# Kernel tuning notes

Hardware: AMD Instinct MI355X
Metric: run time of the kernel (lower is better)

Reference implementation:

```python
import jax, jax.numpy as jnp
import numpy as np

B, C, H, W = 8, 256, 128, 128
N = H * W
TEMP = 0.07
NUM_NEG = 128
HARD_RADIUS = 4
HARD_RATIO = 0.75   # curriculum fully ramped (_current_hard_ratio == hard_ratio_max)
N_HARD = int(NUM_NEG * HARD_RATIO)   # 96
N_RAND = NUM_NEG - N_HARD            # 32
STEP = max(1, H // 16)               # 8
N_POS = ((H + STEP - 1) // STEP) * ((W + STEP - 1) // STEP)  # 256


def setup_inputs() -> dict:
    key = jax.random.key(0)
    ks = jax.random.split(key, 8)
    fmap_rgb = jax.random.normal(ks[0], (B, C, H, W), jnp.float32)
    fmap_depth = jax.random.normal(ks[1], (B, C, H, W), jnp.float32)
    pu = jax.random.uniform(ks[2], (B, H, W), jnp.float32) * (W - 1)
    pv = jax.random.uniform(ks[3], (B, H, W), jnp.float32) * (H - 1)
    projected_coords = jnp.stack([pu, pv], axis=1)  # (B,2,H,W)
    valid_mask = (jax.random.uniform(ks[4], (B, H, W)) < 0.9).astype(jnp.float32)
    rand_idx = jax.random.randint(ks[5], (B, N_RAND), 0, N, dtype=jnp.int32)
    hard_off_u = jax.random.randint(ks[6], (B, N_HARD, N_POS), -HARD_RADIUS, HARD_RADIUS + 1, dtype=jnp.int32)
    hard_off_v = jax.random.randint(ks[7], (B, N_HARD, N_POS), -HARD_RADIUS, HARD_RADIUS + 1, dtype=jnp.int32)
    return {
        'fmap_rgb': fmap_rgb, 'fmap_depth': fmap_depth,
        'projected_coords': projected_coords, 'valid_mask': valid_mask,
        'rand_idx': rand_idx, 'hard_off_u': hard_off_u, 'hard_off_v': hard_off_v,
    }


def _normalize(x):
    # F.normalize(dim=1): x / max(||x||_2, eps)
    n = jnp.sqrt(jnp.sum(x * x, axis=1, keepdims=True))
    return x / jnp.maximum(n, 1e-12)


def _bilinear_sample(f, x, y):
    # grid_sample(mode=bilinear, padding=zeros, align_corners=True); unnormalized
    # coords equal pixel coords (x=proj_u, y=proj_v). f:(B,C,H,W), x,y:(B,H,W) -> (B,C,N)
    Bb, Cc, Hh, Ww = f.shape
    ff = f.reshape(Bb, Cc, Hh * Ww)
    xf = x.reshape(Bb, -1)
    yf = y.reshape(Bb, -1)
    x0 = jnp.floor(xf)
    y0 = jnp.floor(yf)
    wx = xf - x0
    wy = yf - y0
    x0i = x0.astype(jnp.int32)
    y0i = y0.astype(jnp.int32)

    def g(ix, iy):
        valid = (ix >= 0) & (ix < Ww) & (iy >= 0) & (iy < Hh)
        idx = jnp.clip(iy, 0, Hh - 1) * Ww + jnp.clip(ix, 0, Ww - 1)
        v = jnp.take_along_axis(ff, idx[:, None, :], axis=2)
        return v * valid[:, None, :]

    return (((1 - wx) * (1 - wy))[:, None, :] * g(x0i, y0i)
            + (wx * (1 - wy))[:, None, :] * g(x0i + 1, y0i)
            + ((1 - wx) * wy)[:, None, :] * g(x0i, y0i + 1)
            + (wx * wy)[:, None, :] * g(x0i + 1, y0i + 1))


def reference(fmap_rgb, fmap_depth, projected_coords, valid_mask, rand_idx, hard_off_u, hard_off_v):
    rgb = _normalize(fmap_rgb)
    dep = _normalize(fmap_depth)
    proj_u = projected_coords[:, 0]
    proj_v = projected_coords[:, 1]

    rgb_pos = _bilinear_sample(rgb, proj_u, proj_v)        # (B,C,N)
    dep_flat = dep.reshape(B, C, N)
    rgb_flat = rgb.reshape(B, C, N)
    pos_sim = jnp.sum(dep_flat * rgb_pos, axis=1) / TEMP    # (B,N)

    # random negatives via gather + batched matmul
    rgb_rand = jnp.take_along_axis(rgb_flat, rand_idx[:, None, :].astype(jnp.int32), axis=2)  # (B,C,n_rand)
    rand_neg = jnp.einsum('bcn,bck->bkn', dep_flat, rgb_rand) / TEMP  # (B,n_rand,N)

    # hard negatives on coarse grid (step = H//16)
    gh = jnp.arange(0, H, STEP)
    gw = jnp.arange(0, W, STEP)
    ghf, gwf = [a.reshape(-1) for a in jnp.meshgrid(gh, gw, indexing='ij')]
    grid_idx = ghf * W + gwf                                # (n_pos,)
    pos_u = jnp.clip(proj_u[:, ghf, gwf], 0, W - 1).astype(jnp.int32)  # (B,n_pos)
    pos_v = jnp.clip(proj_v[:, ghf, gwf], 0, H - 1).astype(jnp.int32)
    off_u = jnp.where((hard_off_u == 0) & (hard_off_v == 0), 1, hard_off_u)
    hu = jnp.clip(pos_u[:, None, :] + off_u, 0, W - 1)      # (B,n_hard,n_pos)
    hv = jnp.clip(pos_v[:, None, :] + hard_off_v, 0, H - 1)
    hard_idx = (hv * W + hu).reshape(B, -1)                 # (B, n_hard*n_pos)
    rgb_hard = jnp.take_along_axis(rgb_flat, hard_idx[:, None, :], axis=2).reshape(B, C, N_HARD, N_POS)
    dep_grid = dep_flat[:, :, grid_idx]                     # (B,C,n_pos)
    hard_sim = jnp.einsum('bcp,bchp->bhp', dep_grid, rgb_hard) / TEMP  # (B,n_hard,n_pos)

    # logsumexp over [pos; random negs; hard negs] -- hard negs only exist at grid
    # positions (the torch code scatters into a dense -inf (B,n_hard,N) tensor;
    # logaddexp at grid positions is mathematically identical and avoids it).
    lse_base = jax.scipy.special.logsumexp(
        jnp.concatenate([pos_sim[:, None, :], rand_neg], axis=1), axis=1)  # (B,N)
    lse_hard = jax.scipy.special.logsumexp(hard_sim, axis=1)               # (B,n_pos)
    lse = lse_base.at[:, grid_idx].set(jnp.logaddexp(lse_base[:, grid_idx], lse_hard))

    mask = valid_mask.reshape(B, N)
    denom = jnp.maximum(jnp.sum(mask), 1.0)
    loss = jnp.sum((lse - pos_sim) * mask) / denom

    # accuracy (no_grad in torch); max over all negatives, hard ones only at grid idx
    max_neg = jnp.max(rand_neg, axis=1)
    max_neg = max_neg.at[:, grid_idx].max(jnp.max(hard_sim, axis=1))
    correct = ((pos_sim > max_neg) & (mask > 0.5)).astype(jnp.float32)
    accuracy = jnp.sum(correct) / denom * 100.0
    return loss, jax.lax.stop_gradient(accuracy)
```

## Files before the change

kernel.cpp:

```cpp
#include <hip/hip_runtime.h>
#include <cfloat>
#include <math.h>

#define B_ 8
#define C_ 256
#define C2_ (C_/2)
#define H_ 128
#define W_ 128
#define N_ (H_*W_)
#define NRAND 32
#define NHARD 96
#define NPOS 256
#define INV_TEMP (1.0f/0.07f)

typedef __attribute__((ext_vector_type(8))) short short8;
typedef __attribute__((ext_vector_type(4))) float f32x4;

__device__ __forceinline__ unsigned bf16rne(float x) {
    unsigned u = __float_as_uint(x);
    return (u + 0x7FFFu + ((u >> 16) & 1u)) >> 16;
}
__device__ __forceinline__ float blo(unsigned w) { return __uint_as_float(w << 16); }
__device__ __forceinline__ float bhi(unsigned w) { return __uint_as_float(w & 0xFFFF0000u); }

__global__ __launch_bounds__(256) void k1_rgb_norm_T(const float* __restrict__ rgb,
                                                     unsigned* __restrict__ rgbT) {
    __shared__ __align__(16) uint4 bounce[64 * 32];
    __shared__ float red[4][64];
    __shared__ float invn[64];
    int bi = blockIdx.x;
    int b  = bi >> 8;
    int p0 = (bi & 255) << 6;
    int t  = threadIdx.x;
    int lane = t & 63, w = t >> 6;

    const float* src = rgb + (size_t)b * C_ * N_ + p0 + lane;
    float v[64];
    float ssq = 0.f;
    #pragma unroll
    for (int k = 0; k < 64; ++k) {
        v[k] = src[(size_t)(w * 64 + k) * N_];
        ssq += v[k] * v[k];
    }
    red[w][lane] = ssq;
    __syncthreads();
    if (t < 64) {
        float s = red[0][t] + red[1][t] + red[2][t] + red[3][t];
        invn[t] = 1.0f / fmaxf(sqrtf(s), 1e-12f);
    }
    __syncthreads();
    float sc = invn[lane];
    int swz = lane & 7;
    #pragma unroll
    for (int j = 0; j < 8; ++j) {
        uint4 q;
        q.x = bf16rne(v[8 * j + 0] * sc) | (bf16rne(v[8 * j + 1] * sc) << 16);
        q.y = bf16rne(v[8 * j + 2] * sc) | (bf16rne(v[8 * j + 3] * sc) << 16);
        q.z = bf16rne(v[8 * j + 4] * sc) | (bf16rne(v[8 * j + 5] * sc) << 16);
        q.w = bf16rne(v[8 * j + 6] * sc) | (bf16rne(v[8 * j + 7] * sc) << 16);
        bounce[lane * 32 + ((w * 8 + j) ^ swz)] = q;
    }
    __syncthreads();
    uint4* dst = (uint4*)(rgbT + (size_t)(b * N_ + p0) * C2_);
    #pragma unroll
    for (int it = 0; it < 8; ++it) {
        int idx = it * 256 + t;
        int px = idx >> 5, j = idx & 31;
        dst[idx] = bounce[px * 32 + (j ^ (px & 7))];
    }
}

__global__ __launch_bounds__(256) void k2_main(
        const float* __restrict__ dep, const unsigned* __restrict__ rgbT,
        const float* __restrict__ coords, const int* __restrict__ rand_idx,
        float* __restrict__ lse_base, float* __restrict__ pos_out,
        float* __restrict__ maxneg_out, unsigned* __restrict__ depG) {
    __shared__ __align__(16) uint4 dep4[64 * 32];
    __shared__ __align__(16) uint4 rs4[32 * 32];
    __shared__ float red[4][64];
    __shared__ float invn[64];
    int bi = blockIdx.x;
    int b  = bi >> 8;
    int p0 = (bi & 255) << 6;
    int t  = threadIdx.x;
    int lane = t & 63, w = t >> 6;

    #pragma unroll
    for (int it = 0; it < 4; ++it) {
        int flat = it * 256 + t;
        int rn = flat >> 5, c8 = flat & 31;
        int idx = rand_idx[b * NRAND + rn];
        const uint4* src = (const uint4*)(rgbT + (size_t)(b * N_ + idx) * C2_);
        rs4[rn * 32 + (c8 ^ (rn & 7))] = src[c8];
    }

    const float* depb = dep + (size_t)b * C_ * N_ + p0 + lane;
    float ssq = 0.f;
    int psw = lane & 7;
    #pragma unroll 2
    for (int i = 0; i < 8; ++i) {
        int c0 = w * 64 + i * 8;
        float v[8];
        #pragma unroll
        for (int k = 0; k < 8; ++k) {
            v[k] = depb[(size_t)(c0 + k) * N_];
            ssq += v[k] * v[k];
        }
        uint4 q;
        q.x = bf16rne(v[0]) | (bf16rne(v[1]) << 16);
        q.y = bf16rne(v[2]) | (bf16rne(v[3]) << 16);
        q.z = bf16rne(v[4]) | (bf16rne(v[5]) << 16);
        q.w = bf16rne(v[6]) | (bf16rne(v[7]) << 16);
        dep4[lane * 32 + ((w * 8 + i) ^ psw)] = q;
    }
    red[w][lane] = ssq;

    int px = t >> 2, g = t & 3;
    int n  = p0 + px;
    float xf = coords[(size_t)b * 2 * N_ + n];
    float yf = coords[(size_t)b * 2 * N_ + N_ + n];
    float x0 = floorf(xf), y0 = floorf(yf);
    float wx = xf - x0, wy = yf - y0;
    int ix = (int)x0 + (g & 1);
    int iy = (int)y0 + (g >> 1);
    float wgt = ((g & 1) ? wx : 1.f - wx) * ((g & 2) ? wy : 1.f - wy);
    if (ix < 0 || ix >= W_ || iy < 0 || iy >= H_) wgt = 0.f;
    int ixc = min(max(ix, 0), W_ - 1), iyc = min(max(iy, 0), H_ - 1);
    const uint4* nbr4 = (const uint4*)(rgbT + (size_t)(b * N_ + iyc * W_ + ixc) * C2_);

    __syncthreads();
    if (t < 64) {
        float s = red[0][t] + red[1][t] + red[2][t] + red[3][t];
        invn[t] = 1.0f / fmaxf(sqrtf(s), 1e-12f);
    }

    f32x4 acc0 = {0.f, 0.f, 0.f, 0.f};
    f32x4 acc1 = {0.f, 0.f, 0.f, 0.f};
    int l15 = lane & 15, l4 = lane >> 4;
    int pxA = (w << 4) + l15;
    const short8* lds8 = (const short8*)dep4;
    const short8* rnd8 = (const short8*)rs4;
    #pragma unroll
    for (int kc = 0; kc < 8; ++kc) {
        int c8 = kc * 4 + l4;
        short8 a  = lds8[pxA * 32 + (c8 ^ (pxA & 7))];
        short8 b0 = rnd8[l15 * 32 + (c8 ^ (l15 & 7))];
        short8 b1 = rnd8[(16 + l15) * 32 + (c8 ^ (l15 & 7))];
        acc0 = __builtin_amdgcn_mfma_f32_16x16x32_bf16(a, b0, acc0, 0, 0, 0);
        acc1 = __builtin_amdgcn_mfma_f32_16x16x32_bf16(a, b1, acc1, 0, 0, 0);
    }

    float accN = 0.f;
    const uint4* drow = dep4 + (size_t)px * 32;
    int dsw = px & 7;
    #pragma unroll 4
    for (int c8 = 0; c8 < 32; ++c8) {
        uint4 dq = drow[c8 ^ dsw];
        uint4 rq = nbr4[c8];
        accN += blo(dq.x) * blo(rq.x) + bhi(dq.x) * bhi(rq.x)
              + blo(dq.y) * blo(rq.y) + bhi(dq.y) * bhi(rq.y)
              + blo(dq.z) * blo(rq.z) + bhi(dq.z) * bhi(rq.z)
              + blo(dq.w) * blo(rq.w) + bhi(dq.w) * bhi(rq.w);
    }
    __syncthreads();

    float* simsF = (float*)rs4;
    #pragma unroll
    for (int r = 0; r < 4; ++r) {
        int prow = (w << 4) + (l4 << 2) + r;
        int swn = r << 2;
        simsF[prow * 32 + (l15 ^ swn)]        = acc0[r];
        simsF[prow * 32 + (16 + (l15 ^ swn))] = acc1[r];
    }
    __syncthreads();

    float scale = invn[px] * INV_TEMP;
    float pp = accN * wgt;
    pp += __shfl_xor(pp, 1, 4);
    pp += __shfl_xor(pp, 2, 4);
    float pos = pp * scale;
    const float4* sf = (const float4*)simsF;
    int fsw = px & 3;
    float4 ra = sf[px * 8 + ((g * 2) ^ fsw)];
    float4 rb = sf[px * 8 + (((g * 2) ^ fsw) ^ 1)];
    float r[8] = {ra.x, ra.y, ra.z, ra.w, rb.x, rb.y, rb.z, rb.w};
    float ml = -FLT_MAX;
    #pragma unroll
    for (int j = 0; j < 8; ++j) { r[j] *= scale; ml = fmaxf(ml, r[j]); }
    ml = fmaxf(ml, __shfl_xor(ml, 1, 4));
    ml = fmaxf(ml, __shfl_xor(ml, 2, 4));
    float mneg = ml;
    float mall = fmaxf(mneg, pos);
    float se = 0.f;
    #pragma unroll
    for (int j = 0; j < 8; ++j) se += expf(r[j] - mall);
    se += __shfl_xor(se, 1, 4);
    se += __shfl_xor(se, 2, 4);
    if (g == 0) {
        float lse = mall + logf(se + expf(pos - mall));
        size_t o = (size_t)b * N_ + n;
        lse_base[o]   = lse;
        pos_out[o]    = pos;
        maxneg_out[o] = mneg;
    }

    int y = p0 >> 7;
    if ((y & 7) == 0) {
        int m = t >> 5, u = t & 31;
        int gpx = m * 8;
        int gx  = (p0 & 127) + gpx;
        int p   = ((y >> 3) << 4) + (gx >> 3);
        float sc = invn[gpx];
        const unsigned* srow = (const unsigned*)(dep4 + (size_t)gpx * 32);
        int xsw = (gpx & 7) << 2;
        unsigned* dst = depG + (size_t)((b << 8) + p) * 128;
        #pragma unroll
        for (int it = 0; it < 4; ++it) {
            int uu = u + it * 32;
            unsigned wv = srow[uu ^ xsw];
            dst[uu] = bf16rne(blo(wv) * sc) | (bf16rne(bhi(wv) * sc) << 16);
        }
    }
}

__global__ __launch_bounds__(192) void k3_hard(
        const unsigned* __restrict__ depG, const unsigned* __restrict__ rgbT,
        const float* __restrict__ coords, const int* __restrict__ hoffu,
        const int* __restrict__ hoffv, float* __restrict__ lse_hard,
        float* __restrict__ max_hard) {
    __shared__ __align__(16) float dv[256];
    __shared__ float sm_[3], ss_[3];
    int bp = blockIdx.x;
    int b = bp >> 8, p = bp & 255;
    int gy = (p >> 4) * 8, gx = (p & 15) * 8;
    int nn = gy * W_ + gx;
    int t  = threadIdx.x;
    if (t < 128) {
        unsigned wv = depG[(size_t)bp * 128 + t];
        dv[2 * t]     = blo(wv);
        dv[2 * t + 1] = bhi(wv);
    }
    float pu = coords[(size_t)b * 2 * N_ + nn];
    float pv = coords[(size_t)b * 2 * N_ + N_ + nn];
    int iu = (int)fminf(fmaxf(pu, 0.f), (float)(W_ - 1));
    int iv = (int)fminf(fmaxf(pv, 0.f), (float)(H_ - 1));
    int h = t >> 1, half = t & 1;
    int ou = hoffu[((size_t)b * NHARD + h) * NPOS + p];
    int ov = hoffv[((size_t)b * NHARD + h) * NPOS + p];
    __syncthreads();
    if (ou == 0 && ov == 0) ou = 1;
    int hu = min(max(iu + ou, 0), W_ - 1);
    int hv = min(max(iv + ov, 0), H_ - 1);
    const uint4* hvec = (const uint4*)(rgbT + (size_t)(b * N_ + hv * W_ + hu) * C2_)
                        + half * 16;
    const float4* dvv = (const float4*)dv + half * 32;
    float acc = 0.f;
    #pragma unroll 4
    for (int c8 = 0; c8 < 16; ++c8) {
        uint4 q = hvec[c8];
        float4 d0 = dvv[c8 * 2];
        float4 d1 = dvv[c8 * 2 + 1];
        acc += d0.x * blo(q.x) + d0.y * bhi(q.x)
             + d0.z * blo(q.y) + d0.w * bhi(q.y)
             + d1.x * blo(q.z) + d1.y * bhi(q.z)
             + d1.z * blo(q.w) + d1.w * bhi(q.w);
    }
    float sim = (acc + __shfl_xor(acc, 1, 2)) * INV_TEMP;
    float m = sim;
    #pragma unroll
    for (int o = 32; o > 0; o >>= 1) m = fmaxf(m, __shfl_xor(m, o, 64));
    int wid = t >> 6;
    if ((t & 63) == 0) sm_[wid] = m;
    __syncthreads();
    float mm = fmaxf(fmaxf(sm_[0], sm_[1]), sm_[2]);
    float e = (half == 0) ? expf(sim - mm) : 0.f;
    #pragma unroll
    for (int o = 32; o > 0; o >>= 1) e += __shfl_xor(e, o, 64);
    if ((t & 63) == 0) ss_[wid] = e;
    __syncthreads();
    if (t == 0) {
        lse_hard[bp] = mm + logf(ss_[0] + ss_[1] + ss_[2]);
        max_hard[bp] = mm;
    }
}

__global__ __launch_bounds__(256) void k4_reduce(
        const float* __restrict__ lse_base, const float* __restrict__ pos_sim,
        const float* __restrict__ max_neg, const float* __restrict__ mask,
        const float* __restrict__ lse_hard, const float* __restrict__ max_hard,
        float* __restrict__ acc) {
    int i = blockIdx.x * 256 + threadIdx.x;
    float l  = lse_base[i], ps = pos_sim[i], mn = max_neg[i], mk = mask[i];
    int b = i >> 14;
    int n = i & (N_ - 1);
    int y = n >> 7, x = n & 127;
    if (((y & 7) | (x & 7)) == 0) {
        int p = ((y >> 3) << 4) + (x >> 3);
        float lh = lse_hard[(b << 8) + p];
        float mh = max_hard[(b << 8) + p];
        float m = fmaxf(l, lh);
        l  = m + logf(expf(l - m) + expf(lh - m));
        mn = fmaxf(mn, mh);
    }
    float s0 = (l - ps) * mk;
    float s1 = (ps > mn && mk > 0.5f) ? 1.f : 0.f;
    float s2 = mk;
    #pragma unroll
    for (int o = 32; o > 0; o >>= 1) {
        s0 += __shfl_down(s0, o, 64);
        s1 += __shfl_down(s1, o, 64);
        s2 += __shfl_down(s2, o, 64);
    }
    __shared__ float r0[4], r1[4], r2[4];
    int wid = threadIdx.x >> 6;
    if ((threadIdx.x & 63) == 0) { r0[wid] = s0; r1[wid] = s1; r2[wid] = s2; }
    __syncthreads();
    if (threadIdx.x == 0) {
        atomicAdd(&acc[0], r0[0] + r0[1] + r0[2] + r0[3]);
        atomicAdd(&acc[1], r1[0] + r1[1] + r1[2] + r1[3]);
        atomicAdd(&acc[2], r2[0] + r2[1] + r2[2] + r2[3]);
    }
}

__global__ void k5_final(const float* __restrict__ acc, float* __restrict__ out) {
    if (threadIdx.x == 0) {
        float denom = fmaxf(acc[2], 1.0f);
        out[0] = acc[0] / denom;
        out[1] = acc[1] / denom * 100.0f;
    }
}

extern "C" void kernel_launch(void* const* d_in, const int* in_sizes, int n_in,
                              void* d_out, int out_size, void* d_ws, size_t ws_size,
                              hipStream_t stream) {
    const float* rgb     = (const float*)d_in[0];
    const float* dep     = (const float*)d_in[1];
    const float* coords  = (const float*)d_in[2];
    const float* mask    = (const float*)d_in[3];
    const int*   rand_i  = (const int*)d_in[4];
    const int*   hoffu   = (const int*)d_in[5];
    const int*   hoffv   = (const int*)d_in[6];
    float* out = (float*)d_out;
    char*  ws  = (char*)d_ws;

    const size_t RGBT_B = (size_t)B_ * N_ * C_ * 2;
    const size_t PIX_B  = (size_t)B_ * N_ * 4;
    unsigned* rgbT  = (unsigned*)ws;
    float* lse_base = (float*)(ws + RGBT_B);
    float* pos_sim  = (float*)(ws + RGBT_B + PIX_B);
    float* max_neg  = (float*)(ws + RGBT_B + 2 * PIX_B);
    float* lse_hard = (float*)(ws + RGBT_B + 3 * PIX_B);
    float* max_hard = (float*)(ws + RGBT_B + 3 * PIX_B + 8192);
    float* acc      = (float*)(ws + RGBT_B + 3 * PIX_B + 2 * 8192);
    unsigned* depG  = (unsigned*)(ws + RGBT_B + 3 * PIX_B + 2 * 8192 + 1024);

    hipMemsetAsync(acc, 0, 16, stream);
    k1_rgb_norm_T<<<B_ * (N_ / 64), 256, 0, stream>>>(rgb, rgbT);
    k2_main<<<B_ * (N_ / 64), 256, 0, stream>>>(dep, rgbT, coords, rand_i,
                                                lse_base, pos_sim, max_neg, depG);
    k3_hard<<<B_ * NPOS, 192, 0, stream>>>(depG, rgbT, coords, hoffu, hoffv,
                                           lse_hard, max_hard);
    k4_reduce<<<(B_ * N_) / 256, 256, 0, stream>>>(lse_base, pos_sim, max_neg,
                                                   mask, lse_hard, max_hard, acc);
    k5_final<<<1, 64, 0, stream>>>(acc, out);
}
```

Before: 371.8 us.

## Fuse hard-negative, reduction and finalize kernels into one launch

Merges the hard-negative scoring kernel, the per-pixel reduction kernel and the finalize kernel into a single launch. The first 2048 blocks compute hard logsumexp and fold it directly into the grid pixel's contribution, and the remaining 512 blocks reduce the non-grid pixels. A last-block-done atomic counter writes the final loss and accuracy. This removes two kernel launches and the lse_hard/max_hard intermediate round trip, at the cost of 256-thread blocks with a quarter of the threads idle in the hard path and extra atomics.

Result: slower. 471.6 us (+26.8%).

```diff
diff --git a/kernel.cpp b/kernel.cpp
--- a/kernel.cpp
+++ b/kernel.cpp
@@ -223,110 +223,131 @@
     }
 }
 
-__global__ __launch_bounds__(192) void k3_hard(
+__global__ __launch_bounds__(256) void kC_hard_reduce(
         const unsigned* __restrict__ depG, const unsigned* __restrict__ rgbT,
         const float* __restrict__ coords, const int* __restrict__ hoffu,
-        const int* __restrict__ hoffv, float* __restrict__ lse_hard,
-        float* __restrict__ max_hard) {
-    __shared__ __align__(16) float dv[256];
-    __shared__ float sm_[3], ss_[3];
-    int bp = blockIdx.x;
-    int b = bp >> 8, p = bp & 255;
-    int gy = (p >> 4) * 8, gx = (p & 15) * 8;
-    int nn = gy * W_ + gx;
-    int t  = threadIdx.x;
-    if (t < 128) {
-        unsigned wv = depG[(size_t)bp * 128 + t];
-        dv[2 * t]     = blo(wv);
-        dv[2 * t + 1] = bhi(wv);
-    }
-    float pu = coords[(size_t)b * 2 * N_ + nn];
-    float pv = coords[(size_t)b * 2 * N_ + N_ + nn];
-    int iu = (int)fminf(fmaxf(pu, 0.f), (float)(W_ - 1));
-    int iv = (int)fminf(fmaxf(pv, 0.f), (float)(H_ - 1));
-    int h = t >> 1, half = t & 1;
-    int ou = hoffu[((size_t)b * NHARD + h) * NPOS + p];
-    int ov = hoffv[((size_t)b * NHARD + h) * NPOS + p];
-    __syncthreads();
-    if (ou == 0 && ov == 0) ou = 1;
-    int hu = min(max(iu + ou, 0), W_ - 1);
-    int hv = min(max(iv + ov, 0), H_ - 1);
-    const uint4* hvec = (const uint4*)(rgbT + (size_t)(b * N_ + hv * W_ + hu) * C2_)
-                        + half * 16;
-    const float4* dvv = (const float4*)dv + half * 32;
-    float acc = 0.f;
-    #pragma unroll 4
-    for (int c8 = 0; c8 < 16; ++c8) {
-        uint4 q = hvec[c8];
-        float4 d0 = dvv[c8 * 2];
-        float4 d1 = dvv[c8 * 2 + 1];
-        acc += d0.x * blo(q.x) + d0.y * bhi(q.x)
-             + d0.z * blo(q.y) + d0.w * bhi(q.y)
-             + d1.x * blo(q.z) + d1.y * bhi(q.z)
-             + d1.z * blo(q.w) + d1.w * bhi(q.w);
-    }
-    float sim = (acc + __shfl_xor(acc, 1, 2)) * INV_TEMP;
-    float m = sim;
-    #pragma unroll
-    for (int o = 32; o > 0; o >>= 1) m = fmaxf(m, __shfl_xor(m, o, 64));
-    int wid = t >> 6;
-    if ((t & 63) == 0) sm_[wid] = m;
-    __syncthreads();
-    float mm = fmaxf(fmaxf(sm_[0], sm_[1]), sm_[2]);
-    float e = (half == 0) ? expf(sim - mm) : 0.f;
-    #pragma unroll
-    for (int o = 32; o > 0; o >>= 1) e += __shfl_xor(e, o, 64);
-    if ((t & 63) == 0) ss_[wid] = e;
-    __syncthreads();
-    if (t == 0) {
-        lse_hard[bp] = mm + logf(ss_[0] + ss_[1] + ss_[2]);
-        max_hard[bp] = mm;
-    }
-}
-
-__global__ __launch_bounds__(256) void k4_reduce(
-        const float* __restrict__ lse_base, const float* __restrict__ pos_sim,
-        const float* __restrict__ max_neg, const float* __restrict__ mask,
-        const float* __restrict__ lse_hard, const float* __restrict__ max_hard,
-        float* __restrict__ acc) {
-    int i = blockIdx.x * 256 + threadIdx.x;
-    float l  = lse_base[i], ps = pos_sim[i], mn = max_neg[i], mk = mask[i];
-    int b = i >> 14;
-    int n = i & (N_ - 1);
-    int y = n >> 7, x = n & 127;
-    if (((y & 7) | (x & 7)) == 0) {
-        int p = ((y >> 3) << 4) + (x >> 3);
-        float lh = lse_hard[(b << 8) + p];
-        float mh = max_hard[(b << 8) + p];
-        float m = fmaxf(l, lh);
-        l  = m + logf(expf(l - m) + expf(lh - m));
-        mn = fmaxf(mn, mh);
-    }
-    float s0 = (l - ps) * mk;
-    float s1 = (ps > mn && mk > 0.5f) ? 1.f : 0.f;
-    float s2 = mk;
-    #pragma unroll
-    for (int o = 32; o > 0; o >>= 1) {
-        s0 += __shfl_down(s0, o, 64);
-        s1 += __shfl_down(s1, o, 64);
-        s2 += __shfl_down(s2, o, 64);
-    }
-    __shared__ float r0[4], r1[4], r2[4];
-    int wid = threadIdx.x >> 6;
-    if ((threadIdx.x & 63) == 0) { r0[wid] = s0; r1[wid] = s1; r2[wid] = s2; }
-    __syncthreads();
-    if (threadIdx.x == 0) {
-        atomicAdd(&acc[0], r0[0] + r0[1] + r0[2] + r0[3]);
-        atomicAdd(&acc[1], r1[0] + r1[1] + r1[2] + r1[3]);
-        atomicAdd(&acc[2], r2[0] + r2[1] + r2[2] + r2[3]);
-    }
-}
-
-__global__ void k5_final(const float* __restrict__ acc, float* __restrict__ out) {
-    if (threadIdx.x == 0) {
-        float denom = fmaxf(acc[2], 1.0f);
-        out[0] = acc[0] / denom;
-        out[1] = acc[1] / denom * 100.0f;
+        const int* __restrict__ hoffv, const float* __restrict__ lse_base,
+        const float* __restrict__ pos_sim, const float* __restrict__ max_neg,
+        const float* __restrict__ mask, float* __restrict__ acc,
+        float* __restrict__ out) {
+    int t = threadIdx.x;
+    float a0 = 0.f, a1 = 0.f, a2 = 0.f;
+    bool contrib = false;
+
+    if (blockIdx.x < 2048) {
+        __shared__ __align__(16) float dv[256];
+        __shared__ float sm_[4], ss_[4];
+        int bp = blockIdx.x;
+        int b = bp >> 8, p = bp & 255;
+        int gy = (p >> 4) * 8, gx = (p & 15) * 8;
+        int nn = gy * W_ + gx;
+        if (t < 128) {
+            unsigned wv = depG[(size_t)bp * 128 + t];
+            dv[2 * t]     = blo(wv);
+            dv[2 * t + 1] = bhi(wv);
+        }
+        float pu = coords[(size_t)b * 2 * N_ + nn];
+        float pv = coords[(size_t)b * 2 * N_ + N_ + nn];
+        int iu = (int)fminf(fmaxf(pu, 0.f), (float)(W_ - 1));
+        int iv = (int)fminf(fmaxf(pv, 0.f), (float)(H_ - 1));
+        int h = t >> 1, half = t & 1;
+        int ou = 1, ov = 0;
+        if (t < 192) {
+            ou = hoffu[((size_t)b * NHARD + h) * NPOS + p];
+            ov = hoffv[((size_t)b * NHARD + h) * NPOS + p];
+        }
+        __syncthreads();
+        float sim = -FLT_MAX;
+        if (t < 192) {
+            if (ou == 0 && ov == 0) ou = 1;
+            int hu = min(max(iu + ou, 0), W_ - 1);
+            int hv = min(max(iv + ov, 0), H_ - 1);
+            const uint4* hvec = (const uint4*)(rgbT + (size_t)(b * N_ + hv * W_ + hu) * C2_)
+                                + half * 16;
+            const float4* dvv = (const float4*)dv + half * 32;
+            float av = 0.f;
+            #pragma unroll
+            for (int c8 = 0; c8 < 16; ++c8) {
+                uint4 q = hvec[c8];
+                float4 d0 = dvv[c8 * 2];
+                float4 d1 = dvv[c8 * 2 + 1];
+                av += d0.x * blo(q.x) + d0.y * bhi(q.x)
+                    + d0.z * blo(q.y) + d0.w * bhi(q.y)
+                    + d1.x * blo(q.z) + d1.y * bhi(q.z)
+                    + d1.z * blo(q.w) + d1.w * bhi(q.w);
+            }
+            sim = (av + __shfl_xor(av, 1, 2)) * INV_TEMP;
+        }
+        float m = sim;
+        #pragma unroll
+        for (int o = 32; o > 0; o >>= 1) m = fmaxf(m, __shfl_xor(m, o, 64));
+        int wid = t >> 6;
+        if ((t & 63) == 0) sm_[wid] = m;
+        __syncthreads();
+        float mm = fmaxf(fmaxf(sm_[0], sm_[1]), fmaxf(sm_[2], sm_[3]));
+        float e = (t < 192 && half == 0) ? expf(sim - mm) : 0.f;
+        #pragma unroll
+        for (int o = 32; o > 0; o >>= 1) e += __shfl_xor(e, o, 64);
+        if ((t & 63) == 0) ss_[wid] = e;
+        __syncthreads();
+        if (t == 0) {
+            float lh = mm + logf(ss_[0] + ss_[1] + ss_[2] + ss_[3]);
+            float mh = mm;
+            size_t o = (size_t)b * N_ + nn;
+            float l  = lse_base[o], ps = pos_sim[o], mn = max_neg[o], mk = mask[o];
+            float mx = fmaxf(l, lh);
+            l  = mx + logf(expf(l - mx) + expf(lh - mx));
+            mn = fmaxf(mn, mh);
+            a0 = (l - ps) * mk;
+            a1 = (ps > mn && mk > 0.5f) ? 1.f : 0.f;
+            a2 = mk;
+            contrib = true;
+        }
+    } else {
+        int i = (int)(blockIdx.x - 2048) * 256 + t;
+        float l  = lse_base[i], ps = pos_sim[i], mn = max_neg[i], mk = mask[i];
+        int n = i & (N_ - 1);
+        int y = n >> 7, x = n & 127;
+        float s0, s1, s2;
+        if (((y & 7) | (x & 7)) == 0) {
+            s0 = 0.f; s1 = 0.f; s2 = 0.f;
+        } else {
+            s0 = (l - ps) * mk;
+            s1 = (ps > mn && mk > 0.5f) ? 1.f : 0.f;
+            s2 = mk;
+        }
+        #pragma unroll
+        for (int o = 32; o > 0; o >>= 1) {
+            s0 += __shfl_down(s0, o, 64);
+            s1 += __shfl_down(s1, o, 64);
+            s2 += __shfl_down(s2, o, 64);
+        }
+        __shared__ float r0[4], r1[4], r2[4];
+        int wid = t >> 6;
+        if ((t & 63) == 0) { r0[wid] = s0; r1[wid] = s1; r2[wid] = s2; }
+        __syncthreads();
+        if (t == 0) {
+            a0 = r0[0] + r0[1] + r0[2] + r0[3];
+            a1 = r1[0] + r1[1] + r1[2] + r1[3];
+            a2 = r2[0] + r2[1] + r2[2] + r2[3];
+            contrib = true;
+        }
+    }
+
+    if (contrib) {
+        atomicAdd(&acc[0], a0);
+        atomicAdd(&acc[1], a1);
+        atomicAdd(&acc[2], a2);
+        __threadfence();
+        unsigned prev = atomicAdd((unsigned*)&acc[3], 1u);
+        if (prev == gridDim.x - 1) {
+            float t0 = atomicAdd(&acc[0], 0.f);
+            float t1 = atomicAdd(&acc[1], 0.f);
+            float t2 = atomicAdd(&acc[2], 0.f);
+            float denom = fmaxf(t2, 1.0f);
+            out[0] = t0 / denom;
+            out[1] = t1 / denom * 100.0f;
+        }
     }
 }
 
@@ -349,18 +370,14 @@
     float* lse_base = (float*)(ws + RGBT_B);
     float* pos_sim  = (float*)(ws + RGBT_B + PIX_B);
     float* max_neg  = (float*)(ws + RGBT_B + 2 * PIX_B);
-    float* lse_hard = (float*)(ws + RGBT_B + 3 * PIX_B);
-    float* max_hard = (float*)(ws + RGBT_B + 3 * PIX_B + 8192);
-    float* acc      = (float*)(ws + RGBT_B + 3 * PIX_B + 2 * 8192);
-    unsigned* depG  = (unsigned*)(ws + RGBT_B + 3 * PIX_B + 2 * 8192 + 1024);
+    float* acc      = (float*)(ws + RGBT_B + 3 * PIX_B);
+    unsigned* depG  = (unsigned*)(ws + RGBT_B + 3 * PIX_B + 1024);
 
     hipMemsetAsync(acc, 0, 16, stream);
     k1_rgb_norm_T<<<B_ * (N_ / 64), 256, 0, stream>>>(rgb, rgbT);
     k2_main<<<B_ * (N_ / 64), 256, 0, stream>>>(dep, rgbT, coords, rand_i,
                                                 lse_base, pos_sim, max_neg, depG);
-    k3_hard<<<B_ * NPOS, 192, 0, stream>>>(depG, rgbT, coords, hoffu, hoffv,
-                                           lse_hard, max_hard);
-    k4_reduce<<<(B_ * N_) / 256, 256, 0, stream>>>(lse_base, pos_sim, max_neg,
-                                                   mask, lse_hard, max_hard, acc);
-    k5_final<<<1, 64, 0, stream>>>(acc, out);
-}
+    kC_hard_reduce<<<2048 + 512, 256, 0, stream>>>(depG, rgbT, coords, hoffu,
+                                                   hoffv, lse_base, pos_sim,
+                                                   max_neg, mask, acc, out);
+}
```
